# Optimization experiments

Hardware: AMD Instinct MI355X
Metric: run time of the kernel (lower is better)

## Reference

```python
import jax, jax.numpy as jnp
import numpy as np
import math

B, H, N, D = 2, 16, 2048, 64

def setup_inputs() -> dict:
    key = jax.random.key(0)
    kq, kk, kv, kb = jax.random.split(key, 4)
    return {
        "query": jax.random.normal(kq, (B, H, N, D), dtype=jnp.float32),
        "key": jax.random.normal(kk, (B, H, N, D), dtype=jnp.float32),
        "value": jax.random.normal(kv, (B, H, N, D), dtype=jnp.float32),
        "relative_position_bias": jax.random.normal(kb, (H, N, N), dtype=jnp.float32),
    }

def reference(query, key, value, relative_position_bias):
    d = query.shape[-1]
    # scores: [B,H,N,N]
    attn = jnp.einsum("bhnd,bhmd->bhnm", query, key) / jnp.sqrt(jnp.asarray(d, query.dtype))
    attn = attn + relative_position_bias[None]  # broadcast over batch
    attn = jax.nn.softmax(attn, axis=-1)
    # dropout p=0.0 -> identity
    output = jnp.einsum("bhnm,bhmd->bhnd", attn, value)
    return (output, attn)
```

## Files before the change

### kernel.cpp

```cpp
#include <hip/hip_runtime.h>
#include <cstdint>

#define BN 2
#define HN 16
#define NN 2048
#define DD 64
#define KT 64
#define NT (NN / KT)
#define QB 128
#define LDP 72
#define LDF 68
#define KVELEMS ((size_t)BN * HN * NN * DD)

typedef __attribute__((ext_vector_type(8))) short short8;
typedef __attribute__((ext_vector_type(2))) uint32_t uint2v;
typedef __attribute__((ext_vector_type(4))) uint32_t uint4v;
typedef __attribute__((ext_vector_type(4))) float float4v;

static __device__ __forceinline__ uint32_t cvt_pk_bf16(float a, float b){
    uint32_t r;
    asm("v_cvt_pk_bf16_f32 %0, %1, %2" : "=v"(r) : "v"(a), "v"(b));
    return r;
}
static __device__ __forceinline__ unsigned short f2bf1(float a){
    return (unsigned short)(cvt_pk_bf16(a, a) & 0xffffu);
}
static __device__ __forceinline__ short8 pack8(float4v f0, float4v f1){
    uint4v u;
    u[0] = cvt_pk_bf16(f0[0], f0[1]);
    u[1] = cvt_pk_bf16(f0[2], f0[3]);
    u[2] = cvt_pk_bf16(f1[0], f1[1]);
    u[3] = cvt_pk_bf16(f1[2], f1[3]);
    return __builtin_bit_cast(short8, u);
}

static __device__ __forceinline__ float4v mfma_bf16(short8 a, short8 b, float4v c){
    return __builtin_amdgcn_mfma_f32_16x16x32_bf16(a, b, c, 0, 0, 0);
}

static __device__ __forceinline__ void barrier_lds(){
    asm volatile("s_waitcnt lgkmcnt(0)" ::: "memory");
    __builtin_amdgcn_s_barrier();
    asm volatile("" ::: "memory");
}
static __device__ __forceinline__ void lgkm_drain(){
    asm volatile("s_waitcnt lgkmcnt(0)" ::: "memory");
}

__global__ void convert_k_kernel(const float* __restrict__ K,
                                 unsigned short* __restrict__ KW){
    size_t i = ((size_t)blockIdx.x * 256 + threadIdx.x) * 8;
    float4v a = *(const float4v*)(K + i);
    float4v b = *(const float4v*)(K + i + 4);
    uint4v u;
    u[0] = cvt_pk_bf16(a[0], a[1]);
    u[1] = cvt_pk_bf16(a[2], a[3]);
    u[2] = cvt_pk_bf16(b[0], b[1]);
    u[3] = cvt_pk_bf16(b[2], b[3]);
    *(uint4v*)(KW + i) = u;
}

__global__ void transpose_v_kernel(const float* __restrict__ V,
                                   unsigned short* __restrict__ VTW){
    __shared__ unsigned short T[64][72];
    const int bid = blockIdx.x;
    const int bh  = bid >> 5;
    const int ct  = bid & 31;
    const int tid = threadIdx.x;

    const float* src = V + ((size_t)bh * NN + ct * 64) * DD;
    const int srow = tid >> 4;
    const int scol = (tid & 15) << 2;
    #pragma unroll
    for(int i = 0; i < 4; ++i){
        const int row = srow + 16 * i;
        float4v f = *(const float4v*)(src + (size_t)row * DD + scol);
        #pragma unroll
        for(int j = 0; j < 4; ++j)
            T[scol + j][row] = f2bf1(f[j]);
    }
    __syncthreads();
    unsigned short* dst = VTW + (size_t)bh * DD * NN + ct * 64;
    const int d  = tid >> 2;
    const int kc = (tid & 3) << 4;
    *(uint4v*)(dst + (size_t)d * NN + kc)     = *(const uint4v*)&T[d][kc];
    *(uint4v*)(dst + (size_t)d * NN + kc + 8) = *(const uint4v*)&T[d][kc + 8];
}

__launch_bounds__(512, 4)
__global__ void attn_fused_kernel(const float* __restrict__ Q,
                                  const unsigned short* __restrict__ KW,
                                  const float* __restrict__ Bias,
                                  const unsigned short* __restrict__ VTW,
                                  float* __restrict__ Out){
    __shared__ unsigned short Kb[2][KT][LDP];
    __shared__ unsigned short Vt[2][DD][LDP];
    __shared__ float Pb[8][16][LDF];

    const int raw  = blockIdx.x;
    const int slot = raw & 7;
    const int idx  = raw >> 3;
    const int h    = slot * 2 + (idx >> 5);
    const int rem  = idx & 31;
    const int b    = rem & 1;
    const int rt   = rem >> 1;

    const int tid = threadIdx.x;
    const int l   = tid & 63;
    const int w   = tid >> 6;
    const int lg  = l >> 4;
    const int ll  = l & 15;
    const int vc  = ll * 4;

    const int sKrow = tid >> 3;
    const int sKcol = (tid & 7) << 3;

    const int qw = rt * QB + w * 16;
    const size_t bh = (size_t)(b * HN + h);
    const float* Qg = Q + (bh * NN + qw) * DD;
    const unsigned short* KgW = KW  + bh * NN * DD;
    const unsigned short* VgW = VTW + bh * DD * NN;
    const float* BgV = Bias + (size_t)h * NN * NN + (size_t)(qw + lg) * NN + vc;
    const float* BgA = Bias + (size_t)h * NN * NN + (size_t)(qw + ll) * NN + lg * 4;

    short8 qf[2];
    {
        const float* qrow = Qg + (size_t)ll * DD + lg * 8;
        #pragma unroll
        for(int ks = 0; ks < 2; ++ks)
            qf[ks] = pack8(*(const float4v*)(qrow + ks * 32),
                           *(const float4v*)(qrow + ks * 32 + 4));
    }

    float lsum = 0.f;

    float4v bv1[4];
    uint4v kreg;
    kreg = *(const uint4v*)(KgW + (size_t)sKrow * DD + sKcol);
    *(uint4v*)&Kb[0][sKrow][sKcol] = kreg;
    kreg = *(const uint4v*)(KgW + (size_t)(KT + sKrow) * DD + sKcol);
    #pragma unroll
    for(int sub = 0; sub < 4; ++sub)
        bv1[sub] = *(const float4v*)(BgA + sub * 16);
    barrier_lds();

    for(int ct = 0; ct < NT; ++ct){
        const int cur = ct & 1;
        if(ct + 1 < NT)
            *(uint4v*)&Kb[cur ^ 1][sKrow][sKcol] = kreg;
        if(ct + 2 < NT)
            kreg = *(const uint4v*)(KgW + (size_t)((ct+2)*KT + sKrow) * DD + sKcol);

        float4v bvN[4];
        if(ct + 1 < NT){
            #pragma unroll
            for(int sub = 0; sub < 4; ++sub)
                bvN[sub] = *(const float4v*)(BgA + (ct+1)*KT + sub * 16);
        }

        float4v acc[4];
        #pragma unroll
        for(int sub = 0; sub < 4; ++sub) acc[sub] = (float4v){0.f,0.f,0.f,0.f};
        __builtin_amdgcn_s_setprio(1);
        #pragma unroll
        for(int sub = 0; sub < 4; ++sub){
            short8 k0 = *(const short8*)&Kb[cur][sub*16 + ll][lg*8];
            short8 k1 = *(const short8*)&Kb[cur][sub*16 + ll][32 + lg*8];
            acc[sub] = mfma_bf16(k0, qf[0], acc[sub]);
            acc[sub] = mfma_bf16(k1, qf[1], acc[sub]);
        }
        __builtin_amdgcn_s_setprio(0);

        #pragma unroll
        for(int sub = 0; sub < 4; ++sub){
            float e0 = __expf(acc[sub][0] * 0.125f + bv1[sub][0]);
            float e1 = __expf(acc[sub][1] * 0.125f + bv1[sub][1]);
            float e2 = __expf(acc[sub][2] * 0.125f + bv1[sub][2]);
            float e3 = __expf(acc[sub][3] * 0.125f + bv1[sub][3]);
            lsum += (e0 + e1) + (e2 + e3);
        }

        if(ct + 1 < NT){
            #pragma unroll
            for(int sub = 0; sub < 4; ++sub) bv1[sub] = bvN[sub];
        }
        barrier_lds();
    }

    lsum += __shfl_xor(lsum, 16);
    lsum += __shfl_xor(lsum, 32);
    const float rlv = 1.0f / lsum;
    float rl[4];
    #pragma unroll
    for(int r = 0; r < 4; ++r)
        rl[r] = __shfl(rlv, lg*4 + r);

    float4v oacc[4];
    #pragma unroll
    for(int ds = 0; ds < 4; ++ds) oacc[ds] = (float4v){0.f,0.f,0.f,0.f};

    float* attnW = Out + (size_t)BN*HN*NN*DD
                 + (bh * NN + qw + lg) * (size_t)NN + vc;

    float4v bv[4];
    uint4v vreg;
    kreg = *(const uint4v*)(KgW + (size_t)sKrow * DD + sKcol);
    vreg = *(const uint4v*)(VgW + (size_t)sKrow * NN + sKcol);
    *(uint4v*)&Kb[0][sKrow][sKcol] = kreg;
    *(uint4v*)&Vt[0][sKrow][sKcol] = vreg;
    kreg = *(const uint4v*)(KgW + (size_t)(KT + sKrow) * DD + sKcol);
    vreg = *(const uint4v*)(VgW + (size_t)sKrow * NN + KT + sKcol);
    #pragma unroll
    for(int it = 0; it < 4; ++it)
        bv[it] = *(const float4v*)(BgV + (size_t)(it * 4) * NN);
    barrier_lds();

    for(int ct = 0; ct < NT; ++ct){
        const int cur = ct & 1;
        if(ct + 1 < NT){
            *(uint4v*)&Kb[cur ^ 1][sKrow][sKcol] = kreg;
            *(uint4v*)&Vt[cur ^ 1][sKrow][sKcol] = vreg;
        }
        if(ct + 2 < NT){
            kreg = *(const uint4v*)(KgW + (size_t)((ct+2)*KT + sKrow) * DD + sKcol);
            vreg = *(const uint4v*)(VgW + (size_t)sKrow * NN + (ct+2)*KT + sKcol);
        }
        #pragma unroll
        for(int it = 0; it < 4; ++it)
            *(float4v*)&Pb[w][it*4 + lg][vc] = bv[it];
        if(ct + 1 < NT){
            #pragma unroll
            for(int it = 0; it < 4; ++it)
                bv[it] = *(const float4v*)(BgV + (size_t)(it * 4) * NN + (ct+1)*KT);
        }

        float4v acc[4];
        #pragma unroll
        for(int sub = 0; sub < 4; ++sub) acc[sub] = (float4v){0.f,0.f,0.f,0.f};
        __builtin_amdgcn_s_setprio(1);
        #pragma unroll
        for(int sub = 0; sub < 4; ++sub){
            short8 b0 = *(const short8*)&Kb[cur][sub*16 + ll][lg*8];
            short8 b1 = *(const short8*)&Kb[cur][sub*16 + ll][32 + lg*8];
            acc[sub] = mfma_bf16(qf[0], b0, acc[sub]);
            acc[sub] = mfma_bf16(qf[1], b1, acc[sub]);
        }
        __builtin_amdgcn_s_setprio(0);

        #pragma unroll
        for(int sub = 0; sub < 2; ++sub)
            #pragma unroll
            for(int r = 0; r < 4; ++r){
                float sv = acc[sub][r] * 0.125f + Pb[w][lg*4+r][sub*16+ll];
                Pb[w][lg*4+r][sub*16+ll] = __expf(sv) * rl[r];
            }
        lgkm_drain();

        short8 pf0;
        {
            float4v p0 = *(const float4v*)&Pb[w][ll][lg*8];
            float4v p1 = *(const float4v*)&Pb[w][ll][lg*8 + 4];
            pf0 = pack8(p0, p1);
        }
        #pragma unroll
        for(int sub = 2; sub < 4; ++sub)
            #pragma unroll
            for(int r = 0; r < 4; ++r){
                float sv = acc[sub][r] * 0.125f + Pb[w][lg*4+r][sub*16+ll];
                Pb[w][lg*4+r][sub*16+ll] = __expf(sv) * rl[r];
            }

        __builtin_amdgcn_s_setprio(1);
        #pragma unroll
        for(int ds = 0; ds < 4; ++ds){
            short8 v0 = *(const short8*)&Vt[cur][ds*16 + ll][lg*8];
            oacc[ds] = mfma_bf16(pf0, v0, oacc[ds]);
        }
        __builtin_amdgcn_s_setprio(0);
        lgkm_drain();

        short8 pf1;
        {
            float4v p2 = *(const float4v*)&Pb[w][ll][32 + lg*8];
            float4v p3 = *(const float4v*)&Pb[w][ll][32 + lg*8 + 4];
            pf1 = pack8(p2, p3);
        }
        __builtin_amdgcn_s_setprio(1);
        #pragma unroll
        for(int ds = 0; ds < 4; ++ds){
            short8 v1 = *(const short8*)&Vt[cur][ds*16 + ll][32 + lg*8];
            oacc[ds] = mfma_bf16(pf1, v1, oacc[ds]);
        }
        __builtin_amdgcn_s_setprio(0);

        #pragma unroll
        for(int it = 0; it < 4; ++it){
            float4v pv = *(const float4v*)&Pb[w][it*4 + lg][vc];
            *(float4v*)(attnW + (size_t)(it*4) * NN + ct*KT) = pv;
        }

        barrier_lds();
    }

    float* outG = Out + (bh * NN + qw) * (size_t)DD;
    #pragma unroll
    for(int ds = 0; ds < 4; ++ds)
        #pragma unroll
        for(int r = 0; r < 4; ++r)
            outG[(size_t)(lg*4 + r) * DD + ds*16 + ll] = oacc[ds][r];
}

extern "C" void kernel_launch(void* const* d_in, const int* in_sizes, int n_in,
                              void* d_out, int out_size, void* d_ws, size_t ws_size,
                              hipStream_t stream) {
    const float* q    = (const float*)d_in[0];
    const float* k    = (const float*)d_in[1];
    const float* v    = (const float*)d_in[2];
    const float* bias = (const float*)d_in[3];
    float* out = (float*)d_out;
    unsigned short* kw  = (unsigned short*)d_ws;
    unsigned short* vtw = kw + KVELEMS;

    hipLaunchKernelGGL(convert_k_kernel, dim3(KVELEMS / 8 / 256), dim3(256), 0, stream,
                       k, kw);
    hipLaunchKernelGGL(transpose_v_kernel, dim3(BN * HN * (NN / 64)), dim3(256), 0, stream,
                       v, vtw);
    hipLaunchKernelGGL(attn_fused_kernel, dim3(BN * HN * (NN / QB)), dim3(512), 0, stream,
                       q, kw, bias, vtw, out);
}
```

Measured before the change: 288.9 us.

## Swap MFMA operands to transpose accumulator layout, drop bias LDS staging

Swaps the A/B operands of the QK^T and PV MFMAs so each lane holds a row of scores, not a column. Bias is then loaded straight into registers in the matching layout instead of being staged through LDS, and the per-row 1/l value needs no shuffles. Probability tiles and the final output are written as vector float4 stores. This aims to cut LDS traffic, scalar LDS reads and writes, and shuffles in the second pass, at the cost of extra registers for the prefetched bias.

```diff
diff --git a/kernel.cpp b/kernel.cpp
--- a/kernel.cpp
+++ b/kernel.cpp
@@ -120,7 +120,6 @@
     const float* Qg = Q + (bh * NN + qw) * DD;
     const unsigned short* KgW = KW  + bh * NN * DD;
     const unsigned short* VgW = VTW + bh * DD * NN;
-    const float* BgV = Bias + (size_t)h * NN * NN + (size_t)(qw + lg) * NN + vc;
     const float* BgA = Bias + (size_t)h * NN * NN + (size_t)(qw + ll) * NN + lg * 4;
 
     short8 qf[2];
@@ -190,10 +189,6 @@
     lsum += __shfl_xor(lsum, 16);
     lsum += __shfl_xor(lsum, 32);
     const float rlv = 1.0f / lsum;
-    float rl[4];
-    #pragma unroll
-    for(int r = 0; r < 4; ++r)
-        rl[r] = __shfl(rlv, lg*4 + r);
 
     float4v oacc[4];
     #pragma unroll
@@ -202,7 +197,6 @@
     float* attnW = Out + (size_t)BN*HN*NN*DD
                  + (bh * NN + qw + lg) * (size_t)NN + vc;
 
-    float4v bv[4];
     uint4v vreg;
     kreg = *(const uint4v*)(KgW + (size_t)sKrow * DD + sKcol);
     vreg = *(const uint4v*)(VgW + (size_t)sKrow * NN + sKcol);
@@ -211,8 +205,8 @@
     kreg = *(const uint4v*)(KgW + (size_t)(KT + sKrow) * DD + sKcol);
     vreg = *(const uint4v*)(VgW + (size_t)sKrow * NN + KT + sKcol);
     #pragma unroll
-    for(int it = 0; it < 4; ++it)
-        bv[it] = *(const float4v*)(BgV + (size_t)(it * 4) * NN);
+    for(int sub = 0; sub < 4; ++sub)
+        bv1[sub] = *(const float4v*)(BgA + sub * 16);
     barrier_lds();
 
     for(int ct = 0; ct < NT; ++ct){
@@ -225,13 +219,11 @@
             kreg = *(const uint4v*)(KgW + (size_t)((ct+2)*KT + sKrow) * DD + sKcol);
             vreg = *(const uint4v*)(VgW + (size_t)sKrow * NN + (ct+2)*KT + sKcol);
         }
-        #pragma unroll
-        for(int it = 0; it < 4; ++it)
-            *(float4v*)&Pb[w][it*4 + lg][vc] = bv[it];
-        if(ct + 1 < NT){
-            #pragma unroll
-            for(int it = 0; it < 4; ++it)
-                bv[it] = *(const float4v*)(BgV + (size_t)(it * 4) * NN + (ct+1)*KT);
+        float4v bvN[4];
+        if(ct + 1 < NT){
+            #pragma unroll
+            for(int sub = 0; sub < 4; ++sub)
+                bvN[sub] = *(const float4v*)(BgA + (ct+1)*KT + sub * 16);
         }
 
         float4v acc[4];
@@ -240,20 +232,21 @@
         __builtin_amdgcn_s_setprio(1);
         #pragma unroll
         for(int sub = 0; sub < 4; ++sub){
-            short8 b0 = *(const short8*)&Kb[cur][sub*16 + ll][lg*8];
-            short8 b1 = *(const short8*)&Kb[cur][sub*16 + ll][32 + lg*8];
-            acc[sub] = mfma_bf16(qf[0], b0, acc[sub]);
-            acc[sub] = mfma_bf16(qf[1], b1, acc[sub]);
+            short8 k0 = *(const short8*)&Kb[cur][sub*16 + ll][lg*8];
+            short8 k1 = *(const short8*)&Kb[cur][sub*16 + ll][32 + lg*8];
+            acc[sub] = mfma_bf16(k0, qf[0], acc[sub]);
+            acc[sub] = mfma_bf16(k1, qf[1], acc[sub]);
         }
         __builtin_amdgcn_s_setprio(0);
 
         #pragma unroll
-        for(int sub = 0; sub < 2; ++sub)
-            #pragma unroll
-            for(int r = 0; r < 4; ++r){
-                float sv = acc[sub][r] * 0.125f + Pb[w][lg*4+r][sub*16+ll];
-                Pb[w][lg*4+r][sub*16+ll] = __expf(sv) * rl[r];
-            }
+        for(int sub = 0; sub < 2; ++sub){
+            float4v p4;
+            #pragma unroll
+            for(int r = 0; r < 4; ++r)
+                p4[r] = __expf(acc[sub][r] * 0.125f + bv1[sub][r]) * rlv;
+            *(float4v*)&Pb[w][ll][sub*16 + lg*4] = p4;
+        }
         lgkm_drain();
 
         short8 pf0;
@@ -263,18 +256,19 @@
             pf0 = pack8(p0, p1);
         }
         #pragma unroll
-        for(int sub = 2; sub < 4; ++sub)
-            #pragma unroll
-            for(int r = 0; r < 4; ++r){
-                float sv = acc[sub][r] * 0.125f + Pb[w][lg*4+r][sub*16+ll];
-                Pb[w][lg*4+r][sub*16+ll] = __expf(sv) * rl[r];
-            }
+        for(int sub = 2; sub < 4; ++sub){
+            float4v p4;
+            #pragma unroll
+            for(int r = 0; r < 4; ++r)
+                p4[r] = __expf(acc[sub][r] * 0.125f + bv1[sub][r]) * rlv;
+            *(float4v*)&Pb[w][ll][sub*16 + lg*4] = p4;
+        }
 
         __builtin_amdgcn_s_setprio(1);
         #pragma unroll
         for(int ds = 0; ds < 4; ++ds){
             short8 v0 = *(const short8*)&Vt[cur][ds*16 + ll][lg*8];
-            oacc[ds] = mfma_bf16(pf0, v0, oacc[ds]);
+            oacc[ds] = mfma_bf16(v0, pf0, oacc[ds]);
         }
         __builtin_amdgcn_s_setprio(0);
         lgkm_drain();
@@ -289,25 +283,27 @@
         #pragma unroll
         for(int ds = 0; ds < 4; ++ds){
             short8 v1 = *(const short8*)&Vt[cur][ds*16 + ll][32 + lg*8];
-            oacc[ds] = mfma_bf16(pf1, v1, oacc[ds]);
+            oacc[ds] = mfma_bf16(v1, pf1, oacc[ds]);
         }
         __builtin_amdgcn_s_setprio(0);
 
         #pragma unroll
         for(int it = 0; it < 4; ++it){
-            float4v pv = *(const float4v*)&Pb[w][it*4 + lg][vc];
+            float4v pv = *(const float4v*)&Pb[w][lg + 4*it][vc];
             *(float4v*)(attnW + (size_t)(it*4) * NN + ct*KT) = pv;
         }
 
+        if(ct + 1 < NT){
+            #pragma unroll
+            for(int sub = 0; sub < 4; ++sub) bv1[sub] = bvN[sub];
+        }
         barrier_lds();
     }
 
     float* outG = Out + (bh * NN + qw) * (size_t)DD;
     #pragma unroll
     for(int ds = 0; ds < 4; ++ds)
-        #pragma unroll
-        for(int r = 0; r < 4; ++r)
-            outG[(size_t)(lg*4 + r) * DD + ds*16 + ll] = oacc[ds][r];
+        *(float4v*)(outG + (size_t)ll * DD + ds*16 + lg*4) = oacc[ds];
 }
 
 extern "C" void kernel_launch(void* const* d_in, const int* in_sizes, int n_in,
```

Result: no change. 292.9 us (+1.4%).
